# Kernel tuning notes

Measured on AMD Instinct MI355X. Metric: run time of the kernel, lower is better.

## Reference

```python
import jax, jax.numpy as jnp
import numpy as np

E = 8        # num experts
TOP = 2      # top-k
D = 1024     # emb_size


def setup_inputs() -> dict:
    key = jax.random.key(0)
    ks = jax.random.split(key, 8)
    s = 1.0 / np.sqrt(D)
    x = jax.random.normal(ks[0], (4, 2048, D), dtype=jnp.float32)
    Wg = jax.random.uniform(ks[1], (D, E), jnp.float32, -s, s)
    bg = jax.random.uniform(ks[2], (E,), jnp.float32, -s, s)
    W1 = jax.random.uniform(ks[3], (E, D, D), jnp.float32, -s, s)
    b1 = jax.random.uniform(ks[4], (E, D), jnp.float32, -s, s)
    W2 = jax.random.uniform(ks[5], (E, D, D), jnp.float32, -s, s)
    b2 = jax.random.uniform(ks[6], (E, D), jnp.float32, -s, s)
    return {"x": x, "Wg": Wg, "bg": bg, "W1": W1, "b1": b1, "W2": W2, "b2": b2}


def reference(x, Wg, bg, W1, b1, W2, b2):
    x_shape = x.shape
    xt = x.reshape(-1, x_shape[-1])                       # [N, D] tokens
    gate_prob = jax.nn.softmax(xt @ Wg + bg, axis=-1)     # [N, E]
    top_w, top_i = jax.lax.top_k(gate_prob, TOP)          # [N, TOP]
    top_w = jax.nn.softmax(top_w, axis=-1)                # renormalize over top-k
    N = xt.shape[0]
    # combine weights scattered into dense [N, E] (each token has TOP nonzeros)
    comb = jnp.zeros((N, E), xt.dtype).at[jnp.arange(N)[:, None], top_i].add(top_w)
    # per-expert 2-layer MLP applied to all tokens; masked-out tokens get 0 combine weight
    h = jax.nn.relu(jnp.einsum('nd,edf->enf', xt, W1) + b1[:, None, :])   # [E, N, D]
    ye = jnp.einsum('enf,efg->eng', h, W2) + b2[:, None, :]               # [E, N, D]
    y = jnp.einsum('ne,eng->ng', comb, ye)                                # [N, D]
    return y.reshape(x_shape), gate_prob
```

## Files before the change

### kernel.cpp

```cpp
#include <hip/hip_runtime.h>
#include <stdint.h>

#define TOKENS 8192
#define DIM    1024
#define NEXP   8
#define NASSIGN (TOKENS*2)
#define BK     64

#define C_ROW   16
#define C_TILE  25
#define C_TOTAL 34

#define WS_CTRL  0
#define WS_TOPE  1024
#define WS_TOPW  (WS_TOPE + NASSIGN*4)
#define WS_PTOK  (WS_TOPW + NASSIGN*4)
#define WS_AROW  (WS_PTOK + NASSIGN*4)
#define WS_XB    (WS_AROW + NASSIGN*4)
#define WS_W1T   (WS_XB  + (size_t)TOKENS*DIM*2)
#define WS_W2T   (WS_W1T + (size_t)NEXP*DIM*DIM*2)
#define WS_H     (WS_W2T + (size_t)NEXP*DIM*DIM*2)
#define WS_YE    WS_XB

#define WGLD (DIM + 4)

typedef __attribute__((ext_vector_type(8))) short short8;
typedef __attribute__((ext_vector_type(4))) float floatx4;

__device__ __forceinline__ uint32_t bfr(float f) {
  uint32_t v = __float_as_uint(f);
  return (v + 0x7FFFu + ((v >> 16) & 1u)) >> 16;
}
__device__ __forceinline__ float b2f(uint32_t u) { return __uint_as_float(u << 16); }

__device__ __forceinline__ void load_lds16(const void* g, void* l) {
  __builtin_amdgcn_global_load_lds(
      (const __attribute__((address_space(1))) uint32_t*)g,
      (__attribute__((address_space(3))) uint32_t*)l, 16, 0, 0);
}

__global__ __launch_bounds__(256) void gate_kernel(
    const float* __restrict__ x, const float* __restrict__ Wg,
    const float* __restrict__ bg, float* __restrict__ gate_out,
    int* __restrict__ top_e, float* __restrict__ top_w,
    uint16_t* __restrict__ xb) {
  __shared__ __align__(16) float wgs[NEXP * WGLD];
  int t = threadIdx.x;

  #pragma unroll
  for (int k = 0; k < 32; k++) {
    int i = k * 256 + t;
    float v = Wg[i];
    wgs[(i & 7) * WGLD + (i >> 3)] = v;
  }
  __syncthreads();

  int wave = t >> 6, lane = t & 63;
  int tok = blockIdx.x * 4 + wave;
  const float4* xr = (const float4*)(x + (size_t)tok * DIM);
  uint2* xw = (uint2*)(xb + (size_t)tok * DIM);

  float4 acc[NEXP];
  #pragma unroll
  for (int e = 0; e < NEXP; e++) acc[e] = make_float4(0.f, 0.f, 0.f, 0.f);

  #pragma unroll
  for (int c = 0; c < 4; c++) {
    float4 xv = xr[c * 64 + lane];
    uint2 o;
    o.x = bfr(xv.x) | (bfr(xv.y) << 16);
    o.y = bfr(xv.z) | (bfr(xv.w) << 16);
    xw[c * 64 + lane] = o;
    int d0 = (c * 64 + lane) * 4;
    #pragma unroll
    for (int e = 0; e < NEXP; e++) {
      float4 wv = *(const float4*)&wgs[e * WGLD + d0];
      acc[e].x = fmaf(xv.x, wv.x, acc[e].x);
      acc[e].y = fmaf(xv.y, wv.y, acc[e].y);
      acc[e].z = fmaf(xv.z, wv.z, acc[e].z);
      acc[e].w = fmaf(xv.w, wv.w, acc[e].w);
    }
  }
  float s[NEXP];
  #pragma unroll
  for (int e = 0; e < NEXP; e++) s[e] = (acc[e].x + acc[e].y) + (acc[e].z + acc[e].w);
  #pragma unroll
  for (int off = 32; off > 0; off >>= 1) {
    #pragma unroll
    for (int e = 0; e < NEXP; e++) s[e] += __shfl_xor(s[e], off);
  }
  if (lane == 0) {
    float lg[NEXP], p[NEXP];
    float mx = -1e30f;
    #pragma unroll
    for (int e = 0; e < NEXP; e++) { lg[e] = s[e] + bg[e]; mx = fmaxf(mx, lg[e]); }
    float sum = 0.f;
    #pragma unroll
    for (int e = 0; e < NEXP; e++) { p[e] = expf(lg[e] - mx); sum += p[e]; }
    float inv = 1.f / sum;
    #pragma unroll
    for (int e = 0; e < NEXP; e++) p[e] *= inv;
    float4* go = (float4*)(gate_out + (size_t)tok * NEXP);
    go[0] = make_float4(p[0], p[1], p[2], p[3]);
    go[1] = make_float4(p[4], p[5], p[6], p[7]);
    int i1 = 0;
    #pragma unroll
    for (int e = 1; e < NEXP; e++) if (p[e] > p[i1]) i1 = e;
    int i2 = (i1 == 0) ? 1 : 0;
    #pragma unroll
    for (int e = 0; e < NEXP; e++) if (e != i1 && p[e] > p[i2]) i2 = e;
    float ev = expf(p[i2] - p[i1]);
    float w1 = 1.f / (1.f + ev), w2 = ev / (1.f + ev);
    top_e[2*tok]   = i1; top_e[2*tok+1] = i2;
    top_w[2*tok]   = w1; top_w[2*tok+1] = w2;
  }
}

__global__ __launch_bounds__(256) void prep2_kernel(
    const float* __restrict__ W1, const float* __restrict__ W2,
    uint16_t* __restrict__ W1T, uint16_t* __restrict__ W2T,
    const int* __restrict__ top_e,
    int* __restrict__ ctrl, int* __restrict__ ptok, int* __restrict__ arow) {
  __shared__ __align__(16) char smem[64 * 68 * 2];
  __shared__ int scnt[NEXP];
  __shared__ int rowstart[NEXP];
  int t = threadIdx.x;

  if (blockIdx.x != 0) {
    uint16_t (*tile)[68] = (uint16_t (*)[68])smem;
    int cb = blockIdx.x - 1;
    int m  = cb >> 8;
    int d0 = ((cb >> 4) & 15) * 64, f0 = (cb & 15) * 64;
    const float* src = (m < 8) ? (W1 + (size_t)m*DIM*DIM) : (W2 + (size_t)(m-8)*DIM*DIM);
    uint16_t*    dst = (m < 8) ? (W1T + (size_t)m*DIM*DIM) : (W2T + (size_t)(m-8)*DIM*DIM);
    int col = t & 63, rb = (t >> 6) * 16;
    #pragma unroll
    for (int i = 0; i < 16; i++) {
      int dr = rb + i;
      tile[dr][col] = (uint16_t)bfr(src[(size_t)(d0+dr)*DIM + f0 + col]);
    }
    __syncthreads();
    int dg = t & 15, frb = t >> 4;
    #pragma unroll
    for (int i = 0; i < 4; i++) {
      int fr = frb + i * 16;
      uint32_t b0 = tile[dg*4+0][fr], b1 = tile[dg*4+1][fr];
      uint32_t b2 = tile[dg*4+2][fr], b3 = tile[dg*4+3][fr];
      uint2 v;
      v.x = b0 | (b1 << 16);
      v.y = b2 | (b3 << 16);
      *(uint2*)&dst[(size_t)(f0+fr)*DIM + d0 + dg*4] = v;
    }
    return;
  }

  int* sc = (int*)smem;
  int cnt[NEXP];
  #pragma unroll
  for (int e = 0; e < NEXP; e++) cnt[e] = 0;
  for (int j = 0; j < 64; j++) {
    int e = top_e[t * 64 + j];
    cnt[e]++;
  }
  #pragma unroll
  for (int e = 0; e < NEXP; e++) sc[e * 256 + t] = cnt[e];
  __syncthreads();
  int wave = t >> 6, lane = t & 63;
  for (int ee = wave; ee < NEXP; ee += 4) {
    int running = 0;
    for (int chunk = 0; chunk < 4; chunk++) {
      int idx = ee * 256 + chunk * 64 + lane;
      int v = sc[idx];
      int incl = v;
      #pragma unroll
      for (int off = 1; off < 64; off <<= 1) {
        int u = __shfl_up(incl, off);
        if (lane >= off) incl += u;
      }
      sc[idx] = running + incl - v;
      running += __shfl(incl, 63);
    }
    if (lane == 0) scnt[ee] = running;
  }
  __syncthreads();
  if (t == 0) {
    int rs = 0, ts = 0;
    for (int e = 0; e < NEXP; e++) {
      ctrl[C_ROW + e] = rs;
      ctrl[C_TILE + e] = ts;
      rowstart[e] = rs;
      int c = scnt[e];
      rs += c;
      ts += (c + 127) >> 7;
    }
    ctrl[C_ROW + NEXP] = rs;
    ctrl[C_TILE + NEXP] = ts;
    ctrl[C_TOTAL] = ts;
  }
  __syncthreads();
  int off[NEXP];
  #pragma unroll
  for (int e = 0; e < NEXP; e++) off[e] = rowstart[e] + sc[e * 256 + t];
  for (int j = 0; j < 64; j++) {
    int i = t * 64 + j;
    int e = top_e[i];
    int pos = off[e]++;
    ptok[pos] = i >> 1;
    arow[i] = pos;
  }
}

__device__ __forceinline__ bool sched_map(const int* ctrl, int bid,
                                          int& mtile, int& n0) {
  int total = ctrl[C_TOTAL];
  int spx = (total + 7) >> 3;
  int xcd = bid & 7, j = bid >> 3;
  int slot = j >> 3;
  if (slot >= spx) return false;
  mtile = xcd * spx + slot;
  n0 = (j & 7) * 128;
  return mtile < total;
}

__global__ __launch_bounds__(256, 2) void gemm1_kernel(
    const uint16_t* __restrict__ xb, const uint16_t* __restrict__ w1t,
    const float* __restrict__ b1, const int* __restrict__ ctrl,
    const int* __restrict__ ptok, uint16_t* __restrict__ h) {
  __shared__ __align__(16) uint16_t As[128*BK];
  __shared__ __align__(16) uint16_t Bs[128*BK];
  int mtile, n0;
  if (!sched_map(ctrl, blockIdx.x, mtile, n0)) return;
  int e = 0;
  #pragma unroll
  for (int k = 1; k < NEXP; k++) if (mtile >= ctrl[C_TILE + k]) e = k;
  int row0 = ctrl[C_ROW + e] + (mtile - ctrl[C_TILE + e]) * 128;
  int rend = ctrl[C_ROW + e + 1];

  int t = threadIdx.x, lane = t & 63, w = t >> 6;
  const uint16_t* gA[4];
  const uint16_t* gB[4];
  #pragma unroll
  for (int i = 0; i < 4; i++) {
    int s = i * 256 + t;
    int row = s >> 3, cs = s & 7;
    int gc = cs ^ (row & 7);
    int ar = row0 + row; if (ar > NASSIGN-1) ar = NASSIGN-1;
    int tok = ptok[ar];
    gA[i] = xb  + (size_t)tok * DIM + gc*8;
    gB[i] = w1t + (size_t)e*DIM*DIM + (size_t)(n0 + row)*DIM + gc*8;
  }
  floatx4 acc[4][4];
  #pragma unroll
  for (int mi = 0; mi < 4; mi++)
    #pragma unroll
    for (int ni = 0; ni < 4; ni++) acc[mi][ni] = (floatx4)(0.f);

  int wm = w & 1, wn = w >> 1;
  int l15 = lane & 15, lq = lane >> 4;

  for (int kt = 0; kt < DIM/BK; kt++) {
    #pragma unroll
    for (int i = 0; i < 4; i++) {
      load_lds16(gA[i], &As[(i*256 + t) * 8]);
      load_lds16(gB[i], &Bs[(i*256 + t) * 8]);
      gA[i] += BK; gB[i] += BK;
    }
    __syncthreads();
    #pragma unroll
    for (int ks = 0; ks < 2; ks++) {
      short8 a[4], b[4];
      #pragma unroll
      for (int mi = 0; mi < 4; mi++) {
        int row = wm*64 + mi*16 + l15;
        int slot = (ks*4 + lq) ^ (row & 7);
        a[mi] = *(const short8*)&As[row*BK + slot*8];
      }
      #pragma unroll
      for (int ni = 0; ni < 4; ni++) {
        int row = wn*64 + ni*16 + l15;
        int slot = (ks*4 + lq) ^ (row & 7);
        b[ni] = *(const short8*)&Bs[row*BK + slot*8];
      }
      #pragma unroll
      for (int mi = 0; mi < 4; mi++)
        #pragma unroll
        for (int ni = 0; ni < 4; ni++)
          acc[mi][ni] = __builtin_amdgcn_mfma_f32_16x16x32_bf16(a[mi], b[ni], acc[mi][ni], 0, 0, 0);
    }
    __syncthreads();
  }
  #pragma unroll
  for (int mi = 0; mi < 4; mi++) {
    #pragma unroll
    for (int r = 0; r < 4; r++) {
      int rt = wm*64 + mi*16 + lq*4 + r;
      int ar = row0 + rt;
      if (ar < rend) {
        #pragma unroll
        for (int ni = 0; ni < 4; ni++) {
          int n = n0 + wn*64 + ni*16 + l15;
          float v = acc[mi][ni][r] + b1[e*DIM + n];
          v = fmaxf(v, 0.f);
          h[(size_t)ar*DIM + n] = (uint16_t)bfr(v);
        }
      }
    }
  }
}

__global__ __launch_bounds__(256, 2) void gemm2_kernel(
    const uint16_t* __restrict__ h, const uint16_t* __restrict__ w2t,
    const float* __restrict__ b2, const int* __restrict__ ctrl,
    uint16_t* __restrict__ yeb) {
  __shared__ __align__(16) uint16_t As[128*BK];
  __shared__ __align__(16) uint16_t Bs[128*BK];
  int mtile, n0;
  if (!sched_map(ctrl, blockIdx.x, mtile, n0)) return;
  int e = 0;
  #pragma unroll
  for (int k = 1; k < NEXP; k++) if (mtile >= ctrl[C_TILE + k]) e = k;
  int row0 = ctrl[C_ROW + e] + (mtile - ctrl[C_TILE + e]) * 128;
  int rend = ctrl[C_ROW + e + 1];

  int t = threadIdx.x, lane = t & 63, w = t >> 6;
  const uint16_t* gA[4];
  const uint16_t* gB[4];
  #pragma unroll
  for (int i = 0; i < 4; i++) {
    int s = i * 256 + t;
    int row = s >> 3, cs = s & 7;
    int gc = cs ^ (row & 7);
    int ar = row0 + row; if (ar > NASSIGN-1) ar = NASSIGN-1;
    gA[i] = h   + (size_t)ar * DIM + gc*8;
    gB[i] = w2t + (size_t)e*DIM*DIM + (size_t)(n0 + row)*DIM + gc*8;
  }
  floatx4 acc[4][4];
  #pragma unroll
  for (int mi = 0; mi < 4; mi++)
    #pragma unroll
    for (int ni = 0; ni < 4; ni++) acc[mi][ni] = (floatx4)(0.f);

  int wm = w & 1, wn = w >> 1;
  int l15 = lane & 15, lq = lane >> 4;

  for (int kt = 0; kt < DIM/BK; kt++) {
    #pragma unroll
    for (int i = 0; i < 4; i++) {
      load_lds16(gA[i], &As[(i*256 + t) * 8]);
      load_lds16(gB[i], &Bs[(i*256 + t) * 8]);
      gA[i] += BK; gB[i] += BK;
    }
    __syncthreads();
    #pragma unroll
    for (int ks = 0; ks < 2; ks++) {
      short8 a[4], b[4];
      #pragma unroll
      for (int mi = 0; mi < 4; mi++) {
        int row = wm*64 + mi*16 + l15;
        int slot = (ks*4 + lq) ^ (row & 7);
        a[mi] = *(const short8*)&As[row*BK + slot*8];
      }
      #pragma unroll
      for (int ni = 0; ni < 4; ni++) {
        int row = wn*64 + ni*16 + l15;
        int slot = (ks*4 + lq) ^ (row & 7);
        b[ni] = *(const short8*)&Bs[row*BK + slot*8];
      }
      #pragma unroll
      for (int mi = 0; mi < 4; mi++)
        #pragma unroll
        for (int ni = 0; ni < 4; ni++)
          acc[mi][ni] = __builtin_amdgcn_mfma_f32_16x16x32_bf16(a[mi], b[ni], acc[mi][ni], 0, 0, 0);
    }
    __syncthreads();
  }
  #pragma unroll
  for (int mi = 0; mi < 4; mi++) {
    #pragma unroll
    for (int r = 0; r < 4; r++) {
      int rt = wm*64 + mi*16 + lq*4 + r;
      int ar = row0 + rt;
      if (ar < rend) {
        #pragma unroll
        for (int ni = 0; ni < 4; ni++) {
          int n = n0 + wn*64 + ni*16 + l15;
          float v = acc[mi][ni][r] + b2[e*DIM + n];
          yeb[(size_t)ar*DIM + n] = (uint16_t)bfr(v);
        }
      }
    }
  }
}

__global__ __launch_bounds__(256) void combine_kernel(
    const uint16_t* __restrict__ yeb, const int* __restrict__ arow,
    const float* __restrict__ top_w, float* __restrict__ y) {
  int t = threadIdx.x;
  int tok = blockIdx.x * 2 + (t >> 7);
  int i = t & 127;
  int r0 = arow[2*tok], r1 = arow[2*tok+1];
  float w0 = top_w[2*tok], w1 = top_w[2*tok+1];
  const uint4* a = (const uint4*)(yeb + (size_t)r0 * DIM);
  const uint4* b = (const uint4*)(yeb + (size_t)r1 * DIM);
  uint4 av = a[i], bv = b[i];
  float4* yo = (float4*)(y + (size_t)tok * DIM + i * 8);
  float4 o0, o1;
  o0.x = w0 * b2f(av.x & 0xFFFFu) + w1 * b2f(bv.x & 0xFFFFu);
  o0.y = w0 * b2f(av.x >> 16)     + w1 * b2f(bv.x >> 16);
  o0.z = w0 * b2f(av.y & 0xFFFFu) + w1 * b2f(bv.y & 0xFFFFu);
  o0.w = w0 * b2f(av.y >> 16)     + w1 * b2f(bv.y >> 16);
  o1.x = w0 * b2f(av.z & 0xFFFFu) + w1 * b2f(bv.z & 0xFFFFu);
  o1.y = w0 * b2f(av.z >> 16)     + w1 * b2f(bv.z >> 16);
  o1.z = w0 * b2f(av.w & 0xFFFFu) + w1 * b2f(bv.w & 0xFFFFu);
  o1.w = w0 * b2f(av.w >> 16)     + w1 * b2f(bv.w >> 16);
  yo[0] = o0;
  yo[1] = o1;
}

extern "C" void kernel_launch(void* const* d_in, const int* in_sizes, int n_in,
                              void* d_out, int out_size, void* d_ws, size_t ws_size,
                              hipStream_t stream) {
  const float* x  = (const float*)d_in[0];
  const float* Wg = (const float*)d_in[1];
  const float* bg = (const float*)d_in[2];
  const float* W1 = (const float*)d_in[3];
  const float* b1 = (const float*)d_in[4];
  const float* W2 = (const float*)d_in[5];
  const float* b2 = (const float*)d_in[6];
  float* out = (float*)d_out;
  char* ws = (char*)d_ws;

  int*      ctrl = (int*)(ws + WS_CTRL);
  int*      tope = (int*)(ws + WS_TOPE);
  float*    topw = (float*)(ws + WS_TOPW);
  int*      ptok = (int*)(ws + WS_PTOK);
  int*      arow = (int*)(ws + WS_AROW);
  uint16_t* xb   = (uint16_t*)(ws + WS_XB);
  uint16_t* w1t  = (uint16_t*)(ws + WS_W1T);
  uint16_t* w2t  = (uint16_t*)(ws + WS_W2T);
  uint16_t* hbuf = (uint16_t*)(ws + WS_H);
  uint16_t* yeb  = (uint16_t*)(ws + WS_YE);

  gate_kernel<<<2048, 256, 0, stream>>>(x, Wg, bg, out + (size_t)TOKENS*DIM,
                                        tope, topw, xb);
  prep2_kernel<<<4097, 256, 0, stream>>>(W1, W2, w1t, w2t, tope, ctrl, ptok, arow);
  gemm1_kernel<<<136*8, 256, 0, stream>>>(xb, w1t, b1, ctrl, ptok, hbuf);
  gemm2_kernel<<<136*8, 256, 0, stream>>>(hbuf, w2t, b2, ctrl, yeb);
  combine_kernel<<<TOKENS/2, 256, 0, stream>>>(yeb, arow, topw, out);
}
```

Measured before the change: 281.9 us.

## Split weight conversion across gate and prep kernels; raise GEMM occupancy hint

Weight transpose/bf16 conversion blocks are split so 2304 tiles run inside the gate kernel launch and the remaining 1792 run alongside the routing-scan block in the second prep kernel. This balances work between the two prep launches and lets the memory-bound conversion overlap with gating. Separately, the GEMM kernels' launch bounds go from 2 to 4 blocks per CU, which may force register limits and spills.

```diff
diff --git a/kernel.cpp b/kernel.cpp
--- a/kernel.cpp
+++ b/kernel.cpp
@@ -6,6 +6,9 @@
 #define NEXP   8
 #define NASSIGN (TOKENS*2)
 #define BK     64
+
+#define CONV_A 2304
+#define CONV_B 1792
 
 #define C_ROW   16
 #define C_TILE  25
@@ -39,14 +42,50 @@
       (__attribute__((address_space(3))) uint32_t*)l, 16, 0, 0);
 }
 
-__global__ __launch_bounds__(256) void gate_kernel(
+__device__ __forceinline__ void convw_tile(
+    int cb, const float* __restrict__ W1, const float* __restrict__ W2,
+    uint16_t* __restrict__ W1T, uint16_t* __restrict__ W2T,
+    uint16_t (*tile)[68], int t) {
+  int m  = cb >> 8;
+  int d0 = ((cb >> 4) & 15) * 64, f0 = (cb & 15) * 64;
+  const float* src = (m < 8) ? (W1 + (size_t)m*DIM*DIM) : (W2 + (size_t)(m-8)*DIM*DIM);
+  uint16_t*    dst = (m < 8) ? (W1T + (size_t)m*DIM*DIM) : (W2T + (size_t)(m-8)*DIM*DIM);
+  int col = t & 63, rb = (t >> 6) * 16;
+  #pragma unroll
+  for (int i = 0; i < 16; i++) {
+    int dr = rb + i;
+    tile[dr][col] = (uint16_t)bfr(src[(size_t)(d0+dr)*DIM + f0 + col]);
+  }
+  __syncthreads();
+  int dg = t & 15, frb = t >> 4;
+  #pragma unroll
+  for (int i = 0; i < 4; i++) {
+    int fr = frb + i * 16;
+    uint32_t b0 = tile[dg*4+0][fr], b1 = tile[dg*4+1][fr];
+    uint32_t b2 = tile[dg*4+2][fr], b3 = tile[dg*4+3][fr];
+    uint2 v;
+    v.x = b0 | (b1 << 16);
+    v.y = b2 | (b3 << 16);
+    *(uint2*)&dst[(size_t)(f0+fr)*DIM + d0 + dg*4] = v;
+  }
+}
+
+__global__ __launch_bounds__(256) void prep_a_kernel(
     const float* __restrict__ x, const float* __restrict__ Wg,
     const float* __restrict__ bg, float* __restrict__ gate_out,
     int* __restrict__ top_e, float* __restrict__ top_w,
-    uint16_t* __restrict__ xb) {
-  __shared__ __align__(16) float wgs[NEXP * WGLD];
+    uint16_t* __restrict__ xb,
+    const float* __restrict__ W1, const float* __restrict__ W2,
+    uint16_t* __restrict__ W1T, uint16_t* __restrict__ W2T) {
+  __shared__ __align__(16) char smem[NEXP * WGLD * 4];
   int t = threadIdx.x;
 
+  if (blockIdx.x >= 2048) {
+    convw_tile(blockIdx.x - 2048, W1, W2, W1T, W2T, (uint16_t (*)[68])smem, t);
+    return;
+  }
+
+  float* wgs = (float*)smem;
   #pragma unroll
   for (int k = 0; k < 32; k++) {
     int i = k * 256 + t;
@@ -116,7 +155,7 @@
   }
 }
 
-__global__ __launch_bounds__(256) void prep2_kernel(
+__global__ __launch_bounds__(256) void prep_b_kernel(
     const float* __restrict__ W1, const float* __restrict__ W2,
     uint16_t* __restrict__ W1T, uint16_t* __restrict__ W2T,
     const int* __restrict__ top_e,
@@ -127,30 +166,7 @@
   int t = threadIdx.x;
 
   if (blockIdx.x != 0) {
-    uint16_t (*tile)[68] = (uint16_t (*)[68])smem;
-    int cb = blockIdx.x - 1;
-    int m  = cb >> 8;
-    int d0 = ((cb >> 4) & 15) * 64, f0 = (cb & 15) * 64;
-    const float* src = (m < 8) ? (W1 + (size_t)m*DIM*DIM) : (W2 + (size_t)(m-8)*DIM*DIM);
-    uint16_t*    dst = (m < 8) ? (W1T + (size_t)m*DIM*DIM) : (W2T + (size_t)(m-8)*DIM*DIM);
-    int col = t & 63, rb = (t >> 6) * 16;
-    #pragma unroll
-    for (int i = 0; i < 16; i++) {
-      int dr = rb + i;
-      tile[dr][col] = (uint16_t)bfr(src[(size_t)(d0+dr)*DIM + f0 + col]);
-    }
-    __syncthreads();
-    int dg = t & 15, frb = t >> 4;
-    #pragma unroll
-    for (int i = 0; i < 4; i++) {
-      int fr = frb + i * 16;
-      uint32_t b0 = tile[dg*4+0][fr], b1 = tile[dg*4+1][fr];
-      uint32_t b2 = tile[dg*4+2][fr], b3 = tile[dg*4+3][fr];
-      uint2 v;
-      v.x = b0 | (b1 << 16);
-      v.y = b2 | (b3 << 16);
-      *(uint2*)&dst[(size_t)(f0+fr)*DIM + d0 + dg*4] = v;
-    }
+    convw_tile(CONV_A + blockIdx.x - 1, W1, W2, W1T, W2T, (uint16_t (*)[68])smem, t);
     return;
   }
 
@@ -222,7 +238,7 @@
   return mtile < total;
 }
 
-__global__ __launch_bounds__(256, 2) void gemm1_kernel(
+__global__ __launch_bounds__(256, 4) void gemm1_kernel(
     const uint16_t* __restrict__ xb, const uint16_t* __restrict__ w1t,
     const float* __restrict__ b1, const int* __restrict__ ctrl,
     const int* __restrict__ ptok, uint16_t* __restrict__ h) {
@@ -308,7 +324,7 @@
   }
 }
 
-__global__ __launch_bounds__(256, 2) void gemm2_kernel(
+__global__ __launch_bounds__(256, 4) void gemm2_kernel(
     const uint16_t* __restrict__ h, const uint16_t* __restrict__ w2t,
     const float* __restrict__ b2, const int* __restrict__ ctrl,
     uint16_t* __restrict__ yeb) {
@@ -441,9 +457,10 @@
   uint16_t* hbuf = (uint16_t*)(ws + WS_H);
   uint16_t* yeb  = (uint16_t*)(ws + WS_YE);
 
-  gate_kernel<<<2048, 256, 0, stream>>>(x, Wg, bg, out + (size_t)TOKENS*DIM,
-                                        tope, topw, xb);
-  prep2_kernel<<<4097, 256, 0, stream>>>(W1, W2, w1t, w2t, tope, ctrl, ptok, arow);
+  prep_a_kernel<<<2048 + CONV_A, 256, 0, stream>>>(
+      x, Wg, bg, out + (size_t)TOKENS*DIM, tope, topw, xb, W1, W2, w1t, w2t);
+  prep_b_kernel<<<1 + CONV_B, 256, 0, stream>>>(W1, W2, w1t, w2t, tope,
+                                                ctrl, ptok, arow);
   gemm1_kernel<<<136*8, 256, 0, stream>>>(xb, w1t, b1, ctrl, ptok, hbuf);
   gemm2_kernel<<<136*8, 256, 0, stream>>>(hbuf, w2t, b2, ctrl, yeb);
   combine_kernel<<<TOKENS/2, 256, 0, stream>>>(yeb, arow, topw, out);
```

New measurement: 337.1 us. 19.6% more time.
